# Performance work log

Measured on AMD Instinct MI355X. Metric: run time of the kernel, lower is better.

## Reference

```python
import jax, jax.numpy as jnp
import numpy as np

# dims: N batch, L seq, H heads, d projection_dim, P position_dimension
N, Lq, Lk, H, d, P = 2, 1024, 1024, 8, 64, 1
D = H * d


def _kernel(x):
    # _log_exp_kernel: positive feature map log(1+exp(x)) (softplus)
    return jax.nn.softplus(x)


def setup_inputs() -> dict:
    key = jax.random.key(0)
    ks = jax.random.split(key, 8)
    sc = 1.0 / np.sqrt(D).astype(np.float32)
    return {
        "query": jax.random.normal(ks[0], (N, Lq, D), jnp.float32),
        "key_seq": jax.random.normal(ks[1], (N, Lk, D), jnp.float32),
        "Wq": jax.random.normal(ks[2], (D, D), jnp.float32) * sc,
        "Wk": jax.random.normal(ks[3], (D, D), jnp.float32) * sc,
        "Wv": jax.random.normal(ks[4], (D, D), jnp.float32) * sc,
        "position_coeffs": jax.random.uniform(ks[5], (H, d), jnp.float32, 0.5, 1.5),
        "position_weight": jax.random.normal(ks[6], (H, d, P), jnp.float32) * 1e-3,
        "position_bias": jax.random.normal(ks[7], (H, d), jnp.float32) * 1e-2,
    }


def reference(query, key_seq, Wq, Wk, Wv, position_coeffs, position_weight, position_bias):
    # torch Linear (no bias): y = x @ W.T
    q = _kernel(jnp.einsum('nld,ed->nle', query, Wq).reshape(N, Lq, H, d))
    k = _kernel(jnp.einsum('nld,ed->nle', key_seq, Wk).reshape(N, Lk, H, d))
    v = jnp.einsum('nld,ed->nle', key_seq, Wv).reshape(N, Lk, H, d)
    # (N, H, L, d)
    q = jnp.transpose(q, (0, 2, 1, 3))
    k = jnp.transpose(k, (0, 2, 1, 3))
    v = jnp.transpose(v, (0, 2, 1, 3))

    # default positions: arange, query_offset = 0
    qpos = jnp.broadcast_to(jnp.arange(Lq, dtype=jnp.float32).reshape(1, Lq, 1), (N, Lq, P))
    kpos = jnp.broadcast_to(jnp.arange(Lk, dtype=jnp.float32).reshape(1, Lk, 1), (N, Lk, P))
    pq = jnp.einsum('nlp,hkp->nhlk', qpos, position_weight) + position_bias[None, :, None, :]
    pk = jnp.einsum('nlp,hkp->nhlk', kpos, position_weight)

    coeff = position_coeffs[None, :, None, :]  # (1, H, 1, d)

    def part(f, values):
        # causal (mask_future) linear attention via inclusive cumsum over keys
        Qf = q * f(pq) * coeff           # (N, H, Lq, d)
        Kf = k * f(pk)                   # (N, H, Lk, d)
        S = jnp.cumsum(jnp.einsum('nhkd,nhke->nhkde', Kf, values), axis=2)
        return jnp.einsum('nhqd,nhqde->nhqe', Qf, S)

    num = part(jnp.cos, v) + part(jnp.sin, v)           # (N, H, Lq, d)
    unit = jnp.ones((N, H, Lk, 1), jnp.float32)
    den = part(jnp.cos, unit) + part(jnp.sin, unit)     # (N, H, Lq, 1)
    attn = num / den
    return jnp.transpose(attn, (0, 2, 1, 3)).reshape(N, Lq, D)
```

## Files before the change

kernel.cpp:

```cpp
#include <hip/hip_runtime.h>
#include <cmath>

#define NB    2
#define LSEQ  1024
#define NH    8
#define HD    64
#define DD    512
#define FDIM  128
#define EV    65
#define SEP   80
#define CHUNK 64
#define NC    16
#define NBH   16

typedef short short8 __attribute__((ext_vector_type(8)));
typedef float floatx4 __attribute__((ext_vector_type(4)));
typedef unsigned short ushort;

__device__ __forceinline__ float softplusf(float x) {
  return fmaxf(x, 0.0f) + log1pf(expf(-fabsf(x)));
}

__device__ __forceinline__ ushort f2bf(float f) {
  unsigned u = __float_as_uint(f);
  u += 0x7fffu + ((u >> 16) & 1u);
  return (ushort)(u >> 16);
}

__device__ __forceinline__ short8 cvt8(float4 a, float4 b) {
  short8 r;
  r[0] = (short)f2bf(a.x); r[1] = (short)f2bf(a.y);
  r[2] = (short)f2bf(a.z); r[3] = (short)f2bf(a.w);
  r[4] = (short)f2bf(b.x); r[5] = (short)f2bf(b.y);
  r[6] = (short)f2bf(b.z); r[7] = (short)f2bf(b.w);
  return r;
}

__global__ __launch_bounds__(256) void k_proj(
    const float* __restrict__ Xq, const float* __restrict__ Xkv,
    const float* __restrict__ Wq, const float* __restrict__ Wk,
    const float* __restrict__ Wv, const float* __restrict__ pw,
    const float* __restrict__ pb, const float* __restrict__ pc,
    ushort* __restrict__ Qfb, ushort* __restrict__ Kfb,
    ushort* __restrict__ Vxb)
{
  __shared__ short Al[64][72];
  __shared__ short Bl[64][72];
  const int b = blockIdx.x;
  int m0, e0, pmode;
  const float *X, *W;
  if (b < 256) {
    m0 = (b >> 3) << 6; e0 = (b & 7) << 6;
    X = Xq; W = Wq + (size_t)e0 * DD; pmode = 0;
  } else {
    const int bb = b - 256;
    m0 = (bb >> 4) << 6;
    const int nt = bb & 15;
    e0 = (nt & 7) << 6;
    X = Xkv;
    if (nt < 8) { W = Wk + (size_t)e0 * DD; pmode = 1; }
    else        { W = Wv + (size_t)e0 * DD; pmode = 2; }
  }
  const int tid  = threadIdx.x;
  const int r    = tid >> 2;
  const int ko   = (tid & 3) << 4;
  const int wave = tid >> 6, lane = tid & 63;
  const int quad = lane >> 4, lm = lane & 15;
  const float* Ag = X + (size_t)(m0 + r) * DD + ko;
  const float* Bg = W + (size_t)r * DD + ko;
  float4 a[4], bb4[4];
#pragma unroll
  for (int u = 0; u < 4; ++u) {
    a[u]   = *(const float4*)(Ag + (u << 2));
    bb4[u] = *(const float4*)(Bg + (u << 2));
  }
  floatx4 acc[4] = {};
  for (int k0 = 0; k0 < DD; k0 += 64) {
    __syncthreads();
    *(short8*)&Al[r][ko]     = cvt8(a[0], a[1]);
    *(short8*)&Al[r][ko + 8] = cvt8(a[2], a[3]);
    *(short8*)&Bl[r][ko]     = cvt8(bb4[0], bb4[1]);
    *(short8*)&Bl[r][ko + 8] = cvt8(bb4[2], bb4[3]);
    __syncthreads();
    if (k0 + 64 < DD) {
#pragma unroll
      for (int u = 0; u < 4; ++u) {
        a[u]   = *(const float4*)(Ag + k0 + 64 + (u << 2));
        bb4[u] = *(const float4*)(Bg + k0 + 64 + (u << 2));
      }
    }
#pragma unroll
    for (int ks = 0; ks < 2; ++ks) {
      const short8 af = *(const short8*)&Al[(wave << 4) + lm][(quad << 3) + (ks << 5)];
#pragma unroll
      for (int t = 0; t < 4; ++t) {
        const short8 bf = *(const short8*)&Bl[(t << 4) + lm][(quad << 3) + (ks << 5)];
        acc[t] = __builtin_amdgcn_mfma_f32_16x16x32_bf16(af, bf, acc[t], 0, 0, 0);
      }
    }
  }
#pragma unroll
  for (int t = 0; t < 4; ++t) {
    const int e = e0 + (t << 4) + lm;
    const int h = e >> 6, jj = e & 63;
    if (pmode == 2) {
#pragma unroll
      for (int rg = 0; rg < 4; ++rg) {
        const int m = m0 + (wave << 4) + (quad << 2) + rg;
        const int n = m >> 10, l = m & 1023;
        Vxb[((size_t)(n * NH + h) * LSEQ + l) * HD + jj] = f2bf(acc[t][rg]);
      }
    } else {
      const float pwv = pw[e];
      const float pbv = (pmode == 0) ? pb[e] : 0.0f;
      const float pcv = (pmode == 0) ? pc[e] : 1.0f;
      ushort* base = (pmode == 0) ? Qfb : Kfb;
#pragma unroll
      for (int rg = 0; rg < 4; ++rg) {
        const int m = m0 + (wave << 4) + (quad << 2) + rg;
        const int n = m >> 10, l = m & 1023;
        const float v = softplusf(acc[t][rg]) * pcv;
        const float ang = fmaf((float)l, pwv, pbv);
        ushort* dst = &base[((size_t)(n * NH + h) * LSEQ + l) * FDIM + jj];
        dst[0]  = f2bf(v * __cosf(ang));
        dst[64] = f2bf(v * __sinf(ang));
      }
    }
  }
}

__global__ __launch_bounds__(256) void k_chunk_sums(
    const ushort* __restrict__ Kfb, const ushort* __restrict__ Vxb,
    float* __restrict__ S)
{
  const int blk = blockIdx.x;
  const int bh  = blk >> 5;
  const int c   = (blk >> 1) & (NC - 1);
  const int fh  = blk & 1;
  const int f0  = fh << 6;
  const int t0  = c * CHUNK;
  const int tid  = threadIdx.x;
  const int wave = tid >> 6, lane = tid & 63;
  const int quad = lane >> 4, lm = lane & 15;

  __shared__ short KT[64][72];
  __shared__ short VT[80][72];

  for (int i = tid; i < 64 * 8; i += 256) {
    const int t = i & 63, f8 = (i >> 6) << 3;
    const short8 k8 = *(const short8*)&Kfb[((size_t)bh * LSEQ + t0 + t) * FDIM + f0 + f8];
#pragma unroll
    for (int u = 0; u < 8; ++u) KT[f8 + u][t] = k8[u];
  }
  for (int i = tid; i < 64 * 8; i += 256) {
    const int t = i & 63, e8 = (i >> 6) << 3;
    const short8 v8 = *(const short8*)&Vxb[((size_t)bh * LSEQ + t0 + t) * HD + e8];
#pragma unroll
    for (int u = 0; u < 8; ++u) VT[e8 + u][t] = v8[u];
  }
  if (tid < CHUNK) VT[64][tid] = (short)0x3F80;
  __syncthreads();

  short8 aK[2];
#pragma unroll
  for (int ks = 0; ks < 2; ++ks)
    aK[ks] = *(const short8*)&KT[(wave << 4) + lm][(quad << 3) + (ks << 5)];
  floatx4 acc[5] = {};
#pragma unroll
  for (int nt = 0; nt < 5; ++nt)
#pragma unroll
    for (int ks = 0; ks < 2; ++ks) {
      const short8 bf = *(const short8*)&VT[(nt << 4) + lm][(quad << 3) + (ks << 5)];
      acc[nt] = __builtin_amdgcn_mfma_f32_16x16x32_bf16(aK[ks], bf, acc[nt], 0, 0, 0);
    }

  float* Sb = &S[(size_t)(bh * NC + c) * SEP * FDIM];
#pragma unroll
  for (int nt = 0; nt < 4; ++nt)
#pragma unroll
    for (int rg = 0; rg < 4; ++rg) {
      const int f = f0 + (wave << 4) + (quad << 2) + rg;
      Sb[((nt << 4) + lm) * FDIM + f] = acc[nt][rg];
    }
  if (lm == 0) {
#pragma unroll
    for (int rg = 0; rg < 4; ++rg) {
      const int f = f0 + (wave << 4) + (quad << 2) + rg;
      Sb[64 * FDIM + f] = acc[4][rg];
    }
  }
}

__global__ __launch_bounds__(256) void k_scan(
    const float* __restrict__ S, ushort* __restrict__ PTb)
{
  const int bh = blockIdx.x / 13;
  const int eg = blockIdx.x % 13;
  const size_t cs = (size_t)SEP * FDIM;
  const float* Sg = S + (size_t)bh * NC * cs;
  ushort* Pg = PTb + (size_t)bh * NC * cs;
  for (int i = threadIdx.x; i < 5 * FDIM; i += 256) {
    const int e = eg * 5 + (i >> 7);
    const int f = i & 127;
    const int off = e * FDIM + f;
    float v[NC];
#pragma unroll
    for (int c = 0; c < NC; ++c) v[c] = Sg[(size_t)c * cs + off];
    float s = 0.0f;
#pragma unroll
    for (int c = 0; c < NC; ++c) {
      Pg[(size_t)c * cs + off] = f2bf(s);
      s += v[c];
    }
  }
}

__global__ __launch_bounds__(256) void k_chunk_out(
    const ushort* __restrict__ Qfb, const ushort* __restrict__ Kfb,
    const ushort* __restrict__ Vxb, const ushort* __restrict__ PTb,
    float* __restrict__ Out)
{
  const int c  = blockIdx.x & (NC - 1);
  const int bh = blockIdx.x >> 4;
  const int n  = bh >> 3, h = bh & 7;
  const int t0 = c * CHUNK;
  const int tid  = threadIdx.x;
  const int wave = tid >> 6, lane = tid & 63;
  const int quad = lane >> 4, lm = lane & 15;

  __shared__ short QL[64][128];
  __shared__ short KL[64][128];
  __shared__ short ScL[64][72];
  __shared__ short PT[80][136];
  __shared__ short VT[80][72];
  __shared__ float DenL[64];

  const ushort* Qg = &Qfb[((size_t)bh * LSEQ + t0) * FDIM];
  const ushort* Kg = &Kfb[((size_t)bh * LSEQ + t0) * FDIM];
  for (int i = tid; i < 64 * 16; i += 256) {
    const int r = i >> 4, f8 = (i & 15) << 3;
    *(short8*)&QL[r][f8] = *(const short8*)&Qg[r * FDIM + f8];
    *(short8*)&KL[r][f8] = *(const short8*)&Kg[r * FDIM + f8];
  }
  {
    const ushort* Pg = &PTb[(size_t)(bh * NC + c) * SEP * FDIM];
    for (int i = tid; i < 65 * 16; i += 256) {
      const int e = i >> 4, f8 = (i & 15) << 3;
      *(short8*)&PT[e][f8] = *(const short8*)&Pg[e * FDIM + f8];
    }
  }
  for (int i = tid; i < 64 * 8; i += 256) {
    const int t = i & 63, e8 = (i >> 6) << 3;
    const short8 v8 = *(const short8*)&Vxb[((size_t)bh * LSEQ + t0 + t) * HD + e8];
#pragma unroll
    for (int u = 0; u < 8; ++u) VT[e8 + u][t] = v8[u];
  }
  if (tid < CHUNK) VT[64][tid] = (short)0x3F80;
  __syncthreads();

  short8 aQ[4];
#pragma unroll
  for (int ks = 0; ks < 4; ++ks)
    aQ[ks] = *(const short8*)&QL[(wave << 4) + lm][(quad << 3) + (ks << 5)];

  floatx4 accS[4] = {};
#pragma unroll
  for (int nt = 0; nt < 4; ++nt)
#pragma unroll
    for (int ks = 0; ks < 4; ++ks) {
      const short8 b = *(const short8*)&KL[(nt << 4) + lm][(quad << 3) + (ks << 5)];
      accS[nt] = __builtin_amdgcn_mfma_f32_16x16x32_bf16(aQ[ks], b, accS[nt], 0, 0, 0);
    }
#pragma unroll
  for (int nt = 0; nt < 4; ++nt)
#pragma unroll
    for (int rg = 0; rg < 4; ++rg) {
      const int m = (wave << 4) + (quad << 2) + rg;
      const int t = (nt << 4) + lm;
      ScL[m][t] = (short)((t <= m) ? f2bf(accS[nt][rg]) : 0);
    }

  floatx4 accN[5] = {};
#pragma unroll
  for (int nt = 0; nt < 5; ++nt)
#pragma unroll
    for (int ks = 0; ks < 4; ++ks) {
      const short8 b = *(const short8*)&PT[(nt << 4) + lm][(quad << 3) + (ks << 5)];
      accN[nt] = __builtin_amdgcn_mfma_f32_16x16x32_bf16(aQ[ks], b, accN[nt], 0, 0, 0);
    }

  short8 aS[2];
#pragma unroll
  for (int ks = 0; ks < 2; ++ks)
    aS[ks] = *(const short8*)&ScL[(wave << 4) + lm][(quad << 3) + (ks << 5)];
  floatx4 accV[5] = {};
#pragma unroll
  for (int nt = 0; nt < 5; ++nt)
#pragma unroll
    for (int ks = 0; ks < 2; ++ks) {
      const short8 b = *(const short8*)&VT[(nt << 4) + lm][(quad << 3) + (ks << 5)];
      accV[nt] = __builtin_amdgcn_mfma_f32_16x16x32_bf16(aS[ks], b, accV[nt], 0, 0, 0);
    }

  if (lm == 0) {
#pragma unroll
    for (int rg = 0; rg < 4; ++rg)
      DenL[(wave << 4) + (quad << 2) + rg] = accN[4][rg] + accV[4][rg];
  }

#pragma unroll
  for (int rg = 0; rg < 4; ++rg) {
    const int m = (wave << 4) + (quad << 2) + rg;
    const float rden = 1.0f / DenL[m];
    const int l = t0 + m;
#pragma unroll
    for (int nt = 0; nt < 4; ++nt) {
      const float val = (accN[nt][rg] + accV[nt][rg]) * rden;
      Out[((size_t)(n * LSEQ + l)) * DD + h * HD + (nt << 4) + lm] = val;
    }
  }
}

extern "C" void kernel_launch(void* const* d_in, const int* in_sizes, int n_in,
                              void* d_out, int out_size, void* d_ws, size_t ws_size,
                              hipStream_t stream) {
  (void)in_sizes; (void)n_in; (void)out_size; (void)ws_size;
  const float* query  = (const float*)d_in[0];
  const float* keyseq = (const float*)d_in[1];
  const float* Wq     = (const float*)d_in[2];
  const float* Wk     = (const float*)d_in[3];
  const float* Wv     = (const float*)d_in[4];
  const float* pc     = (const float*)d_in[5];
  const float* pw     = (const float*)d_in[6];
  const float* pb     = (const float*)d_in[7];
  float* out = (float*)d_out;

  ushort* Qfb = (ushort*)d_ws;
  ushort* Kfb = Qfb + (size_t)NBH * LSEQ * FDIM;
  ushort* Vxb = Kfb + (size_t)NBH * LSEQ * FDIM;
  float*  S   = (float*)(Vxb + (size_t)NBH * LSEQ * HD);
  ushort* PTb = (ushort*)(S + (size_t)NBH * NC * SEP * FDIM);

  k_proj      <<<768,          256, 0, stream>>>(query, keyseq, Wq, Wk, Wv, pw, pb, pc, Qfb, Kfb, Vxb);
  k_chunk_sums<<<NBH * NC * 2, 256, 0, stream>>>(Kfb, Vxb, S);
  k_scan      <<<NBH * 13,     256, 0, stream>>>(S, PTb);
  k_chunk_out <<<NBH * NC,     256, 0, stream>>>(Qfb, Kfb, Vxb, PTb, out);
}
```

Measured before the change: 112.6 us.

## Pre-convert projection inputs to bf16 and enlarge projection GEMM tiles to 128x128

A new kernel converts query, key and the three weight matrices to bf16 once, into workspace. The projection GEMM then loads bf16 directly and uses 128x128 tiles, with each wave computing a 32x128 slab. The aim is to cut redundant fp32 loads and per-tile conversion, and to raise operand reuse per LDS load. In exchange it adds a launch plus an extra write/read pass over the inputs, and the grid shrinks from 768 to 192 blocks, which may underfill the 256 CUs.

```diff
diff --git a/kernel.cpp b/kernel.cpp
--- a/kernel.cpp
+++ b/kernel.cpp
@@ -13,6 +13,13 @@
 #define NC    16
 #define NBH   16
 
+#define XQ_OFF  0
+#define XK_OFF  1048576
+#define WQ_OFF  2097152
+#define WK_OFF  2359296
+#define WV_OFF  2621440
+#define CVT_TOTAL 2883584
+
 typedef short short8 __attribute__((ext_vector_type(8)));
 typedef float floatx4 __attribute__((ext_vector_type(4)));
 typedef unsigned short ushort;
@@ -36,95 +43,118 @@
   return r;
 }
 
+__global__ __launch_bounds__(256) void k_cvt(
+    const float* __restrict__ q, const float* __restrict__ k,
+    const float* __restrict__ wq, const float* __restrict__ wk,
+    const float* __restrict__ wv, ushort* __restrict__ o)
+{
+  const int idx = (blockIdx.x * 256 + threadIdx.x) * 8;
+  if (idx >= CVT_TOTAL) return;
+  const float* src; int off;
+  if      (idx < XK_OFF) { src = q;  off = idx; }
+  else if (idx < WQ_OFF) { src = k;  off = idx - XK_OFF; }
+  else if (idx < WK_OFF) { src = wq; off = idx - WQ_OFF; }
+  else if (idx < WV_OFF) { src = wk; off = idx - WK_OFF; }
+  else                   { src = wv; off = idx - WV_OFF; }
+  const float4 a = *(const float4*)(src + off);
+  const float4 b = *(const float4*)(src + off + 4);
+  *(short8*)(o + idx) = cvt8(a, b);
+}
+
 __global__ __launch_bounds__(256) void k_proj(
-    const float* __restrict__ Xq, const float* __restrict__ Xkv,
-    const float* __restrict__ Wq, const float* __restrict__ Wk,
-    const float* __restrict__ Wv, const float* __restrict__ pw,
+    const ushort* __restrict__ XW, const float* __restrict__ pw,
     const float* __restrict__ pb, const float* __restrict__ pc,
     ushort* __restrict__ Qfb, ushort* __restrict__ Kfb,
     ushort* __restrict__ Vxb)
 {
-  __shared__ short Al[64][72];
-  __shared__ short Bl[64][72];
+  __shared__ short Al[128][72];
+  __shared__ short Bl[128][72];
   const int b = blockIdx.x;
   int m0, e0, pmode;
-  const float *X, *W;
-  if (b < 256) {
-    m0 = (b >> 3) << 6; e0 = (b & 7) << 6;
-    X = Xq; W = Wq + (size_t)e0 * DD; pmode = 0;
+  const ushort *X, *W;
+  if (b < 64) {
+    m0 = (b >> 2) << 7; e0 = (b & 3) << 7;
+    X = XW + XQ_OFF; W = XW + WQ_OFF + (size_t)e0 * DD; pmode = 0;
   } else {
-    const int bb = b - 256;
-    m0 = (bb >> 4) << 6;
-    const int nt = bb & 15;
-    e0 = (nt & 7) << 6;
-    X = Xkv;
-    if (nt < 8) { W = Wk + (size_t)e0 * DD; pmode = 1; }
-    else        { W = Wv + (size_t)e0 * DD; pmode = 2; }
+    const int bb = b - 64;
+    m0 = (bb >> 3) << 7;
+    const int nt = bb & 7;
+    e0 = (nt & 3) << 7;
+    X = XW + XK_OFF;
+    if (nt < 4) { W = XW + WK_OFF + (size_t)e0 * DD; pmode = 1; }
+    else        { W = XW + WV_OFF + (size_t)e0 * DD; pmode = 2; }
   }
   const int tid  = threadIdx.x;
-  const int r    = tid >> 2;
-  const int ko   = (tid & 3) << 4;
+  const int r    = tid >> 1;
+  const int ko   = (tid & 1) << 5;
   const int wave = tid >> 6, lane = tid & 63;
   const int quad = lane >> 4, lm = lane & 15;
-  const float* Ag = X + (size_t)(m0 + r) * DD + ko;
-  const float* Bg = W + (size_t)r * DD + ko;
-  float4 a[4], bb4[4];
+  const ushort* Ag = X + (size_t)(m0 + r) * DD + ko;
+  const ushort* Bg = W + (size_t)r * DD + ko;
+  short8 a[4], bs[4];
 #pragma unroll
   for (int u = 0; u < 4; ++u) {
-    a[u]   = *(const float4*)(Ag + (u << 2));
-    bb4[u] = *(const float4*)(Bg + (u << 2));
-  }
-  floatx4 acc[4] = {};
+    a[u]  = *(const short8*)(Ag + (u << 3));
+    bs[u] = *(const short8*)(Bg + (u << 3));
+  }
+  floatx4 acc[2][8] = {};
   for (int k0 = 0; k0 < DD; k0 += 64) {
     __syncthreads();
-    *(short8*)&Al[r][ko]     = cvt8(a[0], a[1]);
-    *(short8*)&Al[r][ko + 8] = cvt8(a[2], a[3]);
-    *(short8*)&Bl[r][ko]     = cvt8(bb4[0], bb4[1]);
-    *(short8*)&Bl[r][ko + 8] = cvt8(bb4[2], bb4[3]);
+#pragma unroll
+    for (int u = 0; u < 4; ++u) {
+      *(short8*)&Al[r][ko + (u << 3)] = a[u];
+      *(short8*)&Bl[r][ko + (u << 3)] = bs[u];
+    }
     __syncthreads();
     if (k0 + 64 < DD) {
 #pragma unroll
       for (int u = 0; u < 4; ++u) {
-        a[u]   = *(const float4*)(Ag + k0 + 64 + (u << 2));
-        bb4[u] = *(const float4*)(Bg + k0 + 64 + (u << 2));
+        a[u]  = *(const short8*)(Ag + k0 + 64 + (u << 3));
+        bs[u] = *(const short8*)(Bg + k0 + 64 + (u << 3));
       }
     }
 #pragma unroll
     for (int ks = 0; ks < 2; ++ks) {
-      const short8 af = *(const short8*)&Al[(wave << 4) + lm][(quad << 3) + (ks << 5)];
-#pragma unroll
-      for (int t = 0; t < 4; ++t) {
-        const short8 bf = *(const short8*)&Bl[(t << 4) + lm][(quad << 3) + (ks << 5)];
-        acc[t] = __builtin_amdgcn_mfma_f32_16x16x32_bf16(af, bf, acc[t], 0, 0, 0);
+      const short8 a0 = *(const short8*)&Al[(wave << 5) + lm][(ks << 5) + (quad << 3)];
+      const short8 a1 = *(const short8*)&Al[(wave << 5) + 16 + lm][(ks << 5) + (quad << 3)];
+#pragma unroll
+      for (int t = 0; t < 8; ++t) {
+        const short8 bf = *(const short8*)&Bl[(t << 4) + lm][(ks << 5) + (quad << 3)];
+        acc[0][t] = __builtin_amdgcn_mfma_f32_16x16x32_bf16(a0, bf, acc[0][t], 0, 0, 0);
+        acc[1][t] = __builtin_amdgcn_mfma_f32_16x16x32_bf16(a1, bf, acc[1][t], 0, 0, 0);
       }
     }
   }
 #pragma unroll
-  for (int t = 0; t < 4; ++t) {
+  for (int t = 0; t < 8; ++t) {
     const int e = e0 + (t << 4) + lm;
     const int h = e >> 6, jj = e & 63;
     if (pmode == 2) {
 #pragma unroll
-      for (int rg = 0; rg < 4; ++rg) {
-        const int m = m0 + (wave << 4) + (quad << 2) + rg;
-        const int n = m >> 10, l = m & 1023;
-        Vxb[((size_t)(n * NH + h) * LSEQ + l) * HD + jj] = f2bf(acc[t][rg]);
-      }
+      for (int mi = 0; mi < 2; ++mi)
+#pragma unroll
+        for (int rg = 0; rg < 4; ++rg) {
+          const int m = m0 + (wave << 5) + (mi << 4) + (quad << 2) + rg;
+          const int n = m >> 10, l = m & 1023;
+          Vxb[((size_t)(n * NH + h) * LSEQ + l) * HD + jj] = f2bf(acc[mi][t][rg]);
+        }
     } else {
       const float pwv = pw[e];
       const float pbv = (pmode == 0) ? pb[e] : 0.0f;
       const float pcv = (pmode == 0) ? pc[e] : 1.0f;
       ushort* base = (pmode == 0) ? Qfb : Kfb;
 #pragma unroll
-      for (int rg = 0; rg < 4; ++rg) {
-        const int m = m0 + (wave << 4) + (quad << 2) + rg;
-        const int n = m >> 10, l = m & 1023;
-        const float v = softplusf(acc[t][rg]) * pcv;
-        const float ang = fmaf((float)l, pwv, pbv);
-        ushort* dst = &base[((size_t)(n * NH + h) * LSEQ + l) * FDIM + jj];
-        dst[0]  = f2bf(v * __cosf(ang));
-        dst[64] = f2bf(v * __sinf(ang));
-      }
+      for (int mi = 0; mi < 2; ++mi)
+#pragma unroll
+        for (int rg = 0; rg < 4; ++rg) {
+          const int m = m0 + (wave << 5) + (mi << 4) + (quad << 2) + rg;
+          const int n = m >> 10, l = m & 1023;
+          const float v = softplusf(acc[mi][t][rg]) * pcv;
+          const float ang = fmaf((float)l, pwv, pbv);
+          ushort* dst = &base[((size_t)(n * NH + h) * LSEQ + l) * FDIM + jj];
+          dst[0]  = f2bf(v * __cosf(ang));
+          dst[64] = f2bf(v * __sinf(ang));
+        }
     }
   }
 }
@@ -335,13 +365,15 @@
   const float* pb     = (const float*)d_in[7];
   float* out = (float*)d_out;
 
-  ushort* Qfb = (ushort*)d_ws;
+  ushort* XWb = (ushort*)d_ws;
+  ushort* Qfb = XWb + CVT_TOTAL;
   ushort* Kfb = Qfb + (size_t)NBH * LSEQ * FDIM;
   ushort* Vxb = Kfb + (size_t)NBH * LSEQ * FDIM;
   float*  S   = (float*)(Vxb + (size_t)NBH * LSEQ * HD);
   ushort* PTb = (ushort*)(S + (size_t)NBH * NC * SEP * FDIM);
 
-  k_proj      <<<768,          256, 0, stream>>>(query, keyseq, Wq, Wk, Wv, pw, pb, pc, Qfb, Kfb, Vxb);
+  k_cvt       <<<(CVT_TOTAL / 8 + 255) / 256, 256, 0, stream>>>(query, keyseq, Wq, Wk, Wv, XWb);
+  k_proj      <<<192,          256, 0, stream>>>(XWb, pw, pb, pc, Qfb, Kfb, Vxb);
   k_chunk_sums<<<NBH * NC * 2, 256, 0, stream>>>(Kfb, Vxb, S);
   k_scan      <<<NBH * 13,     256, 0, stream>>>(S, PTb);
   k_chunk_out <<<NBH * NC,     256, 0, stream>>>(Qfb, Kfb, Vxb, PTb, out);
```

New measurement: 122.6 us. 8.9% more time.
